# Kernel tuning notes

Measured on AMD Instinct MI355X. Metric: run time of the kernel, lower is better.

The kernel has to match this reference:

```python
import jax, jax.numpy as jnp
import numpy as np

T, IN, OUT = 16384, 4096, 4096


def setup_inputs() -> dict:
    key = jax.random.key(0)
    k1, k2, k3, k4, k5 = jax.random.split(key, 5)
    x = jax.random.randint(k1, (T, IN), -128, 128, dtype=jnp.int32)      # int8-valued activations
    weight = jax.random.randint(k2, (OUT, IN), -128, 128, dtype=jnp.int32)  # int8-valued weights
    bias = jax.random.randint(k3, (OUT,), -128, 128, dtype=jnp.int32)    # int8-valued bias
    # requant scales: alpha = a_scale*w_scale/o_scale, beta = b_scale/o_scale
    alpha = jax.random.uniform(k4, (1,), jnp.float32, 1e-4, 1e-3)
    beta = jax.random.uniform(k5, (1,), jnp.float32, 0.5, 1.5)
    return {"x": x, "weight": weight, "bias": bias, "alpha": alpha, "beta": beta}


def reference(x, weight, bias, alpha, beta):
    # INT8 GEMM with int32 accumulation: acc[t,o] = sum_i x[t,i] * W[o,i]
    acc = jnp.einsum('ti,oi->to', x, weight,
                     preferred_element_type=jnp.int32)  # [T, OUT] int32
    # inline dequant + bias + requant epilogue
    y = acc.astype(jnp.float32) * alpha + bias.astype(jnp.float32) * beta
    # round and saturate to int8 output (W8A8B8O8)
    out = jnp.clip(jnp.round(y), -128.0, 127.0).astype(jnp.int8)
    return out
```

## Files before the change

kernel.cpp:

```cpp
#include <hip/hip_runtime.h>
#include <stdint.h>

constexpr int T_DIM   = 16384;
constexpr int IN_DIM  = 4096;
constexpr int OUT_DIM = 4096;

using int32x4 = __attribute__((ext_vector_type(4))) int;

#define GLOAD_LDS16(g, l)                                                     \
    __builtin_amdgcn_global_load_lds(                                         \
        (const __attribute__((address_space(1))) void*)(uintptr_t)(g),        \
        (__attribute__((address_space(3))) void*)(uintptr_t)(l), 16, 0, 0)

__global__ void pack_swz(const int* __restrict__ src, int8_t* __restrict__ dst,
                         int rows, int cols) {
    int64_t tid = (int64_t)blockIdx.x * blockDim.x + threadIdx.x;
    int64_t nchunks = (int64_t)rows * (cols / 16);
    if (tid >= nchunks) return;
    int row  = (int)(tid / (cols / 16));
    int cidx = (int)(tid % (cols / 16));
    const int32x4* s4 =
        reinterpret_cast<const int32x4*>(src + (int64_t)row * cols + (cidx << 4));
    uint32_t p[4];
#pragma unroll
    for (int v = 0; v < 4; ++v) {
        int32x4 t = s4[v];
        p[v] = (uint32_t)(t[0] & 0xff) | ((uint32_t)(t[1] & 0xff) << 8) |
               ((uint32_t)(t[2] & 0xff) << 16) | ((uint32_t)(t[3] & 0xff) << 24);
    }
    int cs = (cidx & ~7) | ((cidx & 7) ^ (row & 7));
    *reinterpret_cast<int32x4*>(dst + (int64_t)row * cols + (cs << 4)) =
        *reinterpret_cast<int32x4*>(p);
}

constexpr int BM = 256, BN = 256, BK = 128;
constexpr int NT    = IN_DIM / BK;
constexpr int ATILE = BM * BK;
constexpr int BUFSZ = 2 * ATILE;

__global__ __launch_bounds__(512, 2)
void gemm_i8_8p(const int8_t* __restrict__ x8, const int8_t* __restrict__ w8,
                const int* __restrict__ bias, const float* __restrict__ alphap,
                const float* __restrict__ betap, int* __restrict__ out) {
    __shared__ __align__(16) int8_t lds[2 * BUFSZ];

    const int tid  = threadIdx.x;
    const int lane = tid & 63;
    const int wid  = tid >> 6;
    const int wr   = wid >> 2;
    const int wc   = wid & 3;

    const int nwg = gridDim.x;
    const int cpx = nwg >> 3;
    const int bid = blockIdx.x;
    const int swz = (bid & 7) * cpx + (bid >> 3);
    const int bm  = swz >> 4;
    const int bn  = swz & 15;
    const int brow = bm * BM;
    const int bcol = bn * BN;

    const float alpha = *alphap;
    const float beta  = *betap;

    const int g = lane >> 4;
    const int r = lane & 15;

    const int8_t* pA[4];
    const int8_t* pB[4];
    int dA[4], dB[4];
#pragma unroll
    for (int l = 0; l < 4; ++l) {
        const int off = l * 8192 + tid * 16;
        const int row = off >> 7, in = off & 127;
        pA[l] = x8 + (int64_t)(brow + row) * IN_DIM + in;
        pB[l] = w8 + (int64_t)(bcol + row) * IN_DIM + in;
        dA[l] = off;
        dB[l] = ATILE + off;
    }

    int aoff[8], boff[4];
#pragma unroll
    for (int m = 0; m < 8; ++m) {
        const int row = wr * 128 + m * 16 + r;
        aoff[m] = row * BK + ((g ^ (row & 7)) << 4);
    }
#pragma unroll
    for (int n = 0; n < 4; ++n) {
        const int row = wc * 64 + n * 16 + r;
        boff[n] = ATILE + row * BK + ((g ^ (row & 7)) << 4);
    }

    int32x4 acc[8][4] = {};

#define STAGE8(DSTB)                                                          \
    do {                                                                      \
        int8_t* nb = lds + (DSTB) * BUFSZ;                                    \
        _Pragma("unroll") for (int l = 0; l < 4; ++l) {                       \
            GLOAD_LDS16(pA[l], nb + dA[l]);                                   \
            GLOAD_LDS16(pB[l], nb + dB[l]);                                   \
            pA[l] += BK; pB[l] += BK;                                         \
        }                                                                     \
    } while (0)

#define TILE(RB, SB, PF, LAST)                                                \
    do {                                                                      \
        const int8_t* rb = lds + (RB) * BUFSZ;                                \
        if (PF) STAGE8(SB);                                                   \
        int32x4 af[8], bf[4];                                                 \
                                                                  \
        _Pragma("unroll") for (int n = 0; n < 4; ++n)                         \
            bf[n] = *reinterpret_cast<const int32x4*>(rb + boff[n]);          \
        _Pragma("unroll") for (int m = 0; m < 8; ++m)                         \
            af[m] = *reinterpret_cast<const int32x4*>(rb + aoff[m]);          \
        __builtin_amdgcn_s_setprio(1);                                        \
        _Pragma("unroll") for (int m = 0; m < 8; ++m)                         \
            _Pragma("unroll") for (int n = 0; n < 4; ++n)                     \
                acc[m][n] = __builtin_amdgcn_mfma_i32_16x16x64_i8(            \
                    af[m], bf[n], acc[m][n], 0, 0, 0);                        \
        __builtin_amdgcn_s_setprio(0);                                        \
                                                     \
        _Pragma("unroll") for (int n = 0; n < 4; ++n)                         \
            bf[n] = *reinterpret_cast<const int32x4*>(rb + (boff[n] ^ 64));   \
        _Pragma("unroll") for (int m = 0; m < 8; ++m)                         \
            af[m] = *reinterpret_cast<const int32x4*>(rb + (aoff[m] ^ 64));   \
        __builtin_amdgcn_s_setprio(1);                                        \
        _Pragma("unroll") for (int m = 0; m < 8; ++m)                         \
            _Pragma("unroll") for (int n = 0; n < 4; ++n)                     \
                acc[m][n] = __builtin_amdgcn_mfma_i32_16x16x64_i8(            \
                    af[m], bf[n], acc[m][n], 0, 0, 0);                        \
        __builtin_amdgcn_s_setprio(0);                                        \
        if (!(LAST)) {                                                        \
            asm volatile("s_waitcnt vmcnt(0)" ::: "memory");                  \
            __builtin_amdgcn_s_barrier();                                     \
            asm volatile("" ::: "memory");                                    \
        }                                                                     \
    } while (0)

    STAGE8(0);
    asm volatile("s_waitcnt vmcnt(0)" ::: "memory");
    __builtin_amdgcn_s_barrier();
    asm volatile("" ::: "memory");

#pragma unroll 1
    for (int tt = 0; tt < NT - 2; tt += 2) {
        TILE(0, 1, true, false);
        TILE(1, 0, true, false);
    }
    TILE(0, 1, true,  false);
    TILE(1, 0, false, true);
#undef TILE
#undef STAGE8

    const int r4 = (lane >> 4) * 4;
    const int cl = lane & 15;
#pragma unroll
    for (int n = 0; n < 4; ++n) {
        const int col = bcol + wc * 64 + n * 16 + cl;
        const float bterm = (float)bias[col] * beta;
#pragma unroll
        for (int m = 0; m < 8; ++m) {
            const int row0 = brow + wr * 128 + m * 16 + r4;
#pragma unroll
            for (int j = 0; j < 4; ++j) {
                float y = (float)acc[m][n][j] * alpha + bterm;
                y = rintf(y);
                y = fminf(fmaxf(y, -128.0f), 127.0f);
                out[(int64_t)(row0 + j) * OUT_DIM + col] = (int)y;
            }
        }
    }
}

__global__ __launch_bounds__(256)
void gemm_i8_fb(const int* __restrict__ x32, const int* __restrict__ w32,
                const int* __restrict__ bias, const float* __restrict__ alphap,
                const float* __restrict__ betap, int* __restrict__ out) {
    constexpr int FBM = 128, FBK = 128;
    __shared__ int8_t lA[FBM * FBK];
    __shared__ int8_t lB[FBM * FBK];

    const int tid  = threadIdx.x;
    const int wid  = tid >> 6;
    const int lane = tid & 63;
    const int nwg = gridDim.x;
    const int cpx = nwg >> 3;
    const int bid = blockIdx.x;
    const int swz = (bid & 7) * cpx + (bid >> 3);
    const int brow = (swz >> 5) * FBM;
    const int bcol = (swz & 31) * FBM;
    const int wr = wid >> 1, wc = wid & 1;
    const float alpha = *alphap;
    const float beta  = *betap;

    int32x4 acc[4][4] = {};
    for (int kt = 0; kt < IN_DIM / FBK; ++kt) {
        const int64_t kbase = (int64_t)kt * FBK;
#pragma unroll
        for (int q = 0; q < 4; ++q) {
            const int off = wid * 4096 + q * 1024 + lane * 16;
            const int row = off >> 7;
            const int k   = off & 127;
            const int* ga = x32 + (int64_t)(brow + row) * IN_DIM + kbase + k;
            const int* gb = w32 + (int64_t)(bcol + row) * IN_DIM + kbase + k;
            uint32_t pa[4], pb[4];
#pragma unroll
            for (int v = 0; v < 4; ++v) {
                int32x4 ta = reinterpret_cast<const int32x4*>(ga)[v];
                int32x4 tb = reinterpret_cast<const int32x4*>(gb)[v];
                pa[v] = (uint32_t)(ta[0] & 0xff) | ((uint32_t)(ta[1] & 0xff) << 8) |
                        ((uint32_t)(ta[2] & 0xff) << 16) | ((uint32_t)(ta[3] & 0xff) << 24);
                pb[v] = (uint32_t)(tb[0] & 0xff) | ((uint32_t)(tb[1] & 0xff) << 8) |
                        ((uint32_t)(tb[2] & 0xff) << 16) | ((uint32_t)(tb[3] & 0xff) << 24);
            }
            const int sc = ((k >> 4) ^ (row & 7)) << 4;
            *reinterpret_cast<int32x4*>(lA + row * FBK + sc) = *reinterpret_cast<int32x4*>(pa);
            *reinterpret_cast<int32x4*>(lB + row * FBK + sc) = *reinterpret_cast<int32x4*>(pb);
        }
        __syncthreads();
#pragma unroll
        for (int ks = 0; ks < 2; ++ks) {
            const int gg = lane >> 4, rr = lane & 15;
            const int lc = ks * 4 + gg;
            int32x4 af[4], bf[4];
#pragma unroll
            for (int m = 0; m < 4; ++m) {
                const int row = wr * 64 + m * 16 + rr;
                af[m] = *reinterpret_cast<const int32x4*>(lA + row * FBK + ((lc ^ (row & 7)) << 4));
            }
#pragma unroll
            for (int n = 0; n < 4; ++n) {
                const int row = wc * 64 + n * 16 + rr;
                bf[n] = *reinterpret_cast<const int32x4*>(lB + row * FBK + ((lc ^ (row & 7)) << 4));
            }
#pragma unroll
            for (int m = 0; m < 4; ++m)
#pragma unroll
                for (int n = 0; n < 4; ++n)
                    acc[m][n] = __builtin_amdgcn_mfma_i32_16x16x64_i8(af[m], bf[n], acc[m][n], 0, 0, 0);
        }
        __syncthreads();
    }
    const int r4 = (lane >> 4) * 4;
    const int cl = lane & 15;
#pragma unroll
    for (int n = 0; n < 4; ++n) {
        const int col = bcol + wc * 64 + n * 16 + cl;
        const float bterm = (float)bias[col] * beta;
#pragma unroll
        for (int m = 0; m < 4; ++m) {
            const int row0 = brow + wr * 64 + m * 16 + r4;
#pragma unroll
            for (int j = 0; j < 4; ++j) {
                float y = (float)acc[m][n][j] * alpha + bterm;
                y = rintf(y);
                y = fminf(fmaxf(y, -128.0f), 127.0f);
                out[(int64_t)(row0 + j) * OUT_DIM + col] = (int)y;
            }
        }
    }
}

extern "C" void kernel_launch(void* const* d_in, const int* in_sizes, int n_in,
                              void* d_out, int out_size, void* d_ws, size_t ws_size,
                              hipStream_t stream) {
    const int*   x     = (const int*)d_in[0];
    const int*   w     = (const int*)d_in[1];
    const int*   bias  = (const int*)d_in[2];
    const float* alpha = (const float*)d_in[3];
    const float* beta  = (const float*)d_in[4];
    int*         out   = (int*)d_out;

    const size_t need = (size_t)T_DIM * IN_DIM + (size_t)OUT_DIM * IN_DIM;

    if (ws_size >= need) {
        int8_t* x8 = (int8_t*)d_ws;
        int8_t* w8 = x8 + (size_t)T_DIM * IN_DIM;
        {
            int64_t nch = (int64_t)T_DIM * (IN_DIM / 16);
            pack_swz<<<(int)((nch + 255) / 256), 256, 0, stream>>>(x, x8, T_DIM, IN_DIM);
        }
        {
            int64_t nch = (int64_t)OUT_DIM * (IN_DIM / 16);
            pack_swz<<<(int)((nch + 255) / 256), 256, 0, stream>>>(w, w8, OUT_DIM, IN_DIM);
        }
        const int grid = (T_DIM / BM) * (OUT_DIM / BN);
        gemm_i8_8p<<<grid, 512, 0, stream>>>(x8, w8, bias, alpha, beta, out);
    } else {
        const int grid = (T_DIM / 128) * (OUT_DIM / 128);
        gemm_i8_fb<<<grid, 256, 0, stream>>>(x, w, bias, alpha, beta, out);
    }
}
```

Baseline: 383.2 us.

## Shrink GEMM tile to 256x128x64 for higher occupancy with matching swizzle

Changes the main int8 GEMM tile from 256x256 with K-step 128 to 256x128 with K-step 64, so each wave holds a 4x4 accumulator grid instead of 8x4. Launch bounds rise to 4 blocks per CU. The pack kernel's LDS bank swizzle is rewritten for 64-byte rows. The aim is to cut LDS and register use so more waves hide latency, at the cost of more barriers, twice as many K iterations, and less data reuse per tile.

```diff
diff --git a/kernel.cpp b/kernel.cpp
--- a/kernel.cpp
+++ b/kernel.cpp
@@ -28,18 +28,19 @@
         p[v] = (uint32_t)(t[0] & 0xff) | ((uint32_t)(t[1] & 0xff) << 8) |
                ((uint32_t)(t[2] & 0xff) << 16) | ((uint32_t)(t[3] & 0xff) << 24);
     }
-    int cs = (cidx & ~7) | ((cidx & 7) ^ (row & 7));
+    int cs = (cidx & ~3) | ((cidx & 3) ^ ((row >> 1) & 3));
     *reinterpret_cast<int32x4*>(dst + (int64_t)row * cols + (cs << 4)) =
         *reinterpret_cast<int32x4*>(p);
 }
 
-constexpr int BM = 256, BN = 256, BK = 128;
-constexpr int NT    = IN_DIM / BK;
-constexpr int ATILE = BM * BK;
-constexpr int BUFSZ = 2 * ATILE;
-
-__global__ __launch_bounds__(512, 2)
-void gemm_i8_8p(const int8_t* __restrict__ x8, const int8_t* __restrict__ w8,
+constexpr int BM = 256, BN = 128, BK = 64;
+constexpr int NT     = IN_DIM / BK;
+constexpr int ATILE  = BM * BK;
+constexpr int BTILE  = BN * BK;
+constexpr int BUFSZ  = ATILE + BTILE;
+
+__global__ __launch_bounds__(512, 4)
+void gemm_i8_oc(const int8_t* __restrict__ x8, const int8_t* __restrict__ w8,
                 const int* __restrict__ bias, const float* __restrict__ alphap,
                 const float* __restrict__ betap, int* __restrict__ out) {
     __shared__ __align__(16) int8_t lds[2 * BUFSZ];
@@ -47,15 +48,15 @@
     const int tid  = threadIdx.x;
     const int lane = tid & 63;
     const int wid  = tid >> 6;
-    const int wr   = wid >> 2;
-    const int wc   = wid & 3;
+    const int wr   = wid >> 1;
+    const int wc   = wid & 1;
 
     const int nwg = gridDim.x;
     const int cpx = nwg >> 3;
     const int bid = blockIdx.x;
     const int swz = (bid & 7) * cpx + (bid >> 3);
-    const int bm  = swz >> 4;
-    const int bn  = swz & 15;
+    const int bm  = swz >> 5;
+    const int bn  = swz & 31;
     const int brow = bm * BM;
     const int bcol = bn * BN;
 
@@ -65,66 +66,48 @@
     const int g = lane >> 4;
     const int r = lane & 15;
 
-    const int8_t* pA[4];
-    const int8_t* pB[4];
-    int dA[4], dB[4];
-#pragma unroll
-    for (int l = 0; l < 4; ++l) {
-        const int off = l * 8192 + tid * 16;
-        const int row = off >> 7, in = off & 127;
-        pA[l] = x8 + (int64_t)(brow + row) * IN_DIM + in;
-        pB[l] = w8 + (int64_t)(bcol + row) * IN_DIM + in;
-        dA[l] = off;
-        dB[l] = ATILE + off;
-    }
-
-    int aoff[8], boff[4];
-#pragma unroll
-    for (int m = 0; m < 8; ++m) {
-        const int row = wr * 128 + m * 16 + r;
-        aoff[m] = row * BK + ((g ^ (row & 7)) << 4);
+    const int offA0 = tid * 16;
+    const int offA1 = 8192 + tid * 16;
+    const int offB  = tid * 16;
+    const int8_t* pA0 = x8 + (int64_t)(brow + (offA0 >> 6)) * IN_DIM + (offA0 & 63);
+    const int8_t* pA1 = x8 + (int64_t)(brow + (offA1 >> 6)) * IN_DIM + (offA1 & 63);
+    const int8_t* pB0 = w8 + (int64_t)(bcol + (offB  >> 6)) * IN_DIM + (offB  & 63);
+    const int dA0 = offA0, dA1 = offA1, dB0 = ATILE + offB;
+
+    int aoff[4], boff[4];
+#pragma unroll
+    for (int m = 0; m < 4; ++m) {
+        const int row = wr * 64 + m * 16 + r;
+        aoff[m] = row * BK + ((g ^ ((row >> 1) & 3)) << 4);
     }
 #pragma unroll
     for (int n = 0; n < 4; ++n) {
         const int row = wc * 64 + n * 16 + r;
-        boff[n] = ATILE + row * BK + ((g ^ (row & 7)) << 4);
-    }
-
-    int32x4 acc[8][4] = {};
-
-#define STAGE8(DSTB)                                                          \
+        boff[n] = ATILE + row * BK + ((g ^ ((row >> 1) & 3)) << 4);
+    }
+
+    int32x4 acc[4][4] = {};
+
+#define STAGE3(DSTB)                                                          \
     do {                                                                      \
         int8_t* nb = lds + (DSTB) * BUFSZ;                                    \
-        _Pragma("unroll") for (int l = 0; l < 4; ++l) {                       \
-            GLOAD_LDS16(pA[l], nb + dA[l]);                                   \
-            GLOAD_LDS16(pB[l], nb + dB[l]);                                   \
-            pA[l] += BK; pB[l] += BK;                                         \
-        }                                                                     \
+        GLOAD_LDS16(pA0, nb + dA0);                                           \
+        GLOAD_LDS16(pA1, nb + dA1);                                           \
+        GLOAD_LDS16(pB0, nb + dB0);                                           \
+        pA0 += BK; pA1 += BK; pB0 += BK;                                      \
     } while (0)
 
 #define TILE(RB, SB, PF, LAST)                                                \
     do {                                                                      \
+        if (PF) STAGE3(SB);                                                   \
         const int8_t* rb = lds + (RB) * BUFSZ;                                \
-        if (PF) STAGE8(SB);                                                   \
-        int32x4 af[8], bf[4];                                                 \
-                                                                  \
+        int32x4 af[4], bf[4];                                                 \
         _Pragma("unroll") for (int n = 0; n < 4; ++n)                         \
             bf[n] = *reinterpret_cast<const int32x4*>(rb + boff[n]);          \
-        _Pragma("unroll") for (int m = 0; m < 8; ++m)                         \
+        _Pragma("unroll") for (int m = 0; m < 4; ++m)                         \
             af[m] = *reinterpret_cast<const int32x4*>(rb + aoff[m]);          \
         __builtin_amdgcn_s_setprio(1);                                        \
-        _Pragma("unroll") for (int m = 0; m < 8; ++m)                         \
-            _Pragma("unroll") for (int n = 0; n < 4; ++n)                     \
-                acc[m][n] = __builtin_amdgcn_mfma_i32_16x16x64_i8(            \
-                    af[m], bf[n], acc[m][n], 0, 0, 0);                        \
-        __builtin_amdgcn_s_setprio(0);                                        \
-                                                     \
-        _Pragma("unroll") for (int n = 0; n < 4; ++n)                         \
-            bf[n] = *reinterpret_cast<const int32x4*>(rb + (boff[n] ^ 64));   \
-        _Pragma("unroll") for (int m = 0; m < 8; ++m)                         \
-            af[m] = *reinterpret_cast<const int32x4*>(rb + (aoff[m] ^ 64));   \
-        __builtin_amdgcn_s_setprio(1);                                        \
-        _Pragma("unroll") for (int m = 0; m < 8; ++m)                         \
+        _Pragma("unroll") for (int m = 0; m < 4; ++m)                         \
             _Pragma("unroll") for (int n = 0; n < 4; ++n)                     \
                 acc[m][n] = __builtin_amdgcn_mfma_i32_16x16x64_i8(            \
                     af[m], bf[n], acc[m][n], 0, 0, 0);                        \
@@ -136,7 +119,7 @@
         }                                                                     \
     } while (0)
 
-    STAGE8(0);
+    STAGE3(0);
     asm volatile("s_waitcnt vmcnt(0)" ::: "memory");
     __builtin_amdgcn_s_barrier();
     asm volatile("" ::: "memory");
@@ -149,7 +132,7 @@
     TILE(0, 1, true,  false);
     TILE(1, 0, false, true);
 #undef TILE
-#undef STAGE8
+#undef STAGE3
 
     const int r4 = (lane >> 4) * 4;
     const int cl = lane & 15;
@@ -158,8 +141,8 @@
         const int col = bcol + wc * 64 + n * 16 + cl;
         const float bterm = (float)bias[col] * beta;
 #pragma unroll
-        for (int m = 0; m < 8; ++m) {
-            const int row0 = brow + wr * 128 + m * 16 + r4;
+        for (int m = 0; m < 4; ++m) {
+            const int row0 = brow + wr * 64 + m * 16 + r4;
 #pragma unroll
             for (int j = 0; j < 4; ++j) {
                 float y = (float)acc[m][n][j] * alpha + bterm;
@@ -284,7 +267,7 @@
             pack_swz<<<(int)((nch + 255) / 256), 256, 0, stream>>>(w, w8, OUT_DIM, IN_DIM);
         }
         const int grid = (T_DIM / BM) * (OUT_DIM / BN);
-        gemm_i8_8p<<<grid, 512, 0, stream>>>(x8, w8, bias, alpha, beta, out);
+        gemm_i8_oc<<<grid, 512, 0, stream>>>(x8, w8, bias, alpha, beta, out);
     } else {
         const int grid = (T_DIM / 128) * (OUT_DIM / 128);
         gemm_i8_fb<<<grid, 256, 0, stream>>>(x, w, bias, alpha, beta, out);
```

After: 418.7 us, median of 4. +9.3%, slower.

## Load pre-packed MFMA-fragment weights directly to registers, halve K tile

Applied to the files above, without the earlier changes.

The weight matrix is now pre-packed into MFMA-fragment order, so each lane loads its B operand straight from global memory into registers with double-buffered prefetch, bypassing LDS. Only the activation tile goes through LDS, and BK is halved to 64 with a matching swizzle, so LDS use per block drops. The aim is to cut LDS traffic and shared-memory bank pressure for B. In exchange there are twice as many barrier-synchronised iterations with less MFMA work per barrier, and each B fragment is reloaded from global/L2 by every block that uses it.

```diff
diff --git a/kernel.cpp b/kernel.cpp
--- a/kernel.cpp
+++ b/kernel.cpp
@@ -12,8 +12,8 @@
         (const __attribute__((address_space(1))) void*)(uintptr_t)(g),        \
         (__attribute__((address_space(3))) void*)(uintptr_t)(l), 16, 0, 0)
 
-__global__ void pack_swz(const int* __restrict__ src, int8_t* __restrict__ dst,
-                         int rows, int cols) {
+__global__ void pack_a(const int* __restrict__ src, int8_t* __restrict__ dst,
+                       int rows, int cols) {
     int64_t tid = (int64_t)blockIdx.x * blockDim.x + threadIdx.x;
     int64_t nchunks = (int64_t)rows * (cols / 16);
     if (tid >= nchunks) return;
@@ -28,21 +28,46 @@
         p[v] = (uint32_t)(t[0] & 0xff) | ((uint32_t)(t[1] & 0xff) << 8) |
                ((uint32_t)(t[2] & 0xff) << 16) | ((uint32_t)(t[3] & 0xff) << 24);
     }
-    int cs = (cidx & ~7) | ((cidx & 7) ^ (row & 7));
+    int cs = (cidx & ~3) | ((cidx & 3) ^ ((row >> 1) & 3));
     *reinterpret_cast<int32x4*>(dst + (int64_t)row * cols + (cs << 4)) =
         *reinterpret_cast<int32x4*>(p);
 }
 
-constexpr int BM = 256, BN = 256, BK = 128;
+__global__ void pack_b(const int* __restrict__ src, int8_t* __restrict__ dst,
+                       int rows, int cols) {
+    int64_t tid = (int64_t)blockIdx.x * blockDim.x + threadIdx.x;
+    int64_t nchunks = (int64_t)rows * (cols / 16);
+    if (tid >= nchunks) return;
+    int o  = (int)(tid / (cols / 16));
+    int kc = (int)(tid % (cols / 16));
+    const int32x4* s4 =
+        reinterpret_cast<const int32x4*>(src + (int64_t)o * cols + (kc << 4));
+    uint32_t p[4];
+#pragma unroll
+    for (int v = 0; v < 4; ++v) {
+        int32x4 t = s4[v];
+        p[v] = (uint32_t)(t[0] & 0xff) | ((uint32_t)(t[1] & 0xff) << 8) |
+               ((uint32_t)(t[2] & 0xff) << 16) | ((uint32_t)(t[3] & 0xff) << 24);
+    }
+    const int o_tile = o >> 4;
+    const int k_tile = kc >> 2;
+    const int g      = kc & 3;
+    const int r      = o & 15;
+    const int64_t off =
+        ((int64_t)o_tile * (cols >> 6) + k_tile) * 1024 + g * 256 + r * 16;
+    *reinterpret_cast<int32x4*>(dst + off) = *reinterpret_cast<int32x4*>(p);
+}
+
+constexpr int BM = 256, BN = 256, BK = 64;
 constexpr int NT    = IN_DIM / BK;
 constexpr int ATILE = BM * BK;
-constexpr int BUFSZ = 2 * ATILE;
+constexpr int NKT   = IN_DIM / 64;
 
 __global__ __launch_bounds__(512, 2)
-void gemm_i8_8p(const int8_t* __restrict__ x8, const int8_t* __restrict__ w8,
+void gemm_i8_bb(const int8_t* __restrict__ x8, const int8_t* __restrict__ w8p,
                 const int* __restrict__ bias, const float* __restrict__ alphap,
                 const float* __restrict__ betap, int* __restrict__ out) {
-    __shared__ __align__(16) int8_t lds[2 * BUFSZ];
+    __shared__ __align__(16) int8_t lds[2 * ATILE];
 
     const int tid  = threadIdx.x;
     const int lane = tid & 63;
@@ -65,69 +90,57 @@
     const int g = lane >> 4;
     const int r = lane & 15;
 
-    const int8_t* pA[4];
+    const int offA0 = tid * 16;
+    const int offA1 = 8192 + tid * 16;
+    const int8_t* pA0 = x8 + (int64_t)(brow + (offA0 >> 6)) * IN_DIM + (offA0 & 63);
+    const int8_t* pA1 = x8 + (int64_t)(brow + (offA1 >> 6)) * IN_DIM + (offA1 & 63);
+    const int dA0 = offA0, dA1 = offA1;
+
     const int8_t* pB[4];
-    int dA[4], dB[4];
-#pragma unroll
-    for (int l = 0; l < 4; ++l) {
-        const int off = l * 8192 + tid * 16;
-        const int row = off >> 7, in = off & 127;
-        pA[l] = x8 + (int64_t)(brow + row) * IN_DIM + in;
-        pB[l] = w8 + (int64_t)(bcol + row) * IN_DIM + in;
-        dA[l] = off;
-        dB[l] = ATILE + off;
-    }
-
-    int aoff[8], boff[4];
+#pragma unroll
+    for (int n = 0; n < 4; ++n) {
+        const int o_tile = (bcol >> 4) + wc * 4 + n;
+        pB[n] = w8p + (int64_t)o_tile * NKT * 1024 + lane * 16;
+    }
+
+    int aoff[8];
 #pragma unroll
     for (int m = 0; m < 8; ++m) {
         const int row = wr * 128 + m * 16 + r;
-        aoff[m] = row * BK + ((g ^ (row & 7)) << 4);
-    }
-#pragma unroll
-    for (int n = 0; n < 4; ++n) {
-        const int row = wc * 64 + n * 16 + r;
-        boff[n] = ATILE + row * BK + ((g ^ (row & 7)) << 4);
+        aoff[m] = row * BK + ((g ^ ((row >> 1) & 3)) << 4);
     }
 
     int32x4 acc[8][4] = {};
-
-#define STAGE8(DSTB)                                                          \
+    int32x4 b0[4], b1[4];
+
+#define STAGE_A(DSTB)                                                         \
     do {                                                                      \
-        int8_t* nb = lds + (DSTB) * BUFSZ;                                    \
-        _Pragma("unroll") for (int l = 0; l < 4; ++l) {                       \
-            GLOAD_LDS16(pA[l], nb + dA[l]);                                   \
-            GLOAD_LDS16(pB[l], nb + dB[l]);                                   \
-            pA[l] += BK; pB[l] += BK;                                         \
+        int8_t* nb = lds + (DSTB) * ATILE;                                    \
+        GLOAD_LDS16(pA0, nb + dA0);                                           \
+        GLOAD_LDS16(pA1, nb + dA1);                                           \
+        pA0 += BK; pA1 += BK;                                                 \
+    } while (0)
+
+#define LOAD_B(DST)                                                           \
+    do {                                                                      \
+        _Pragma("unroll") for (int n = 0; n < 4; ++n) {                       \
+            DST[n] = *reinterpret_cast<const int32x4*>(pB[n]);                \
+            pB[n] += 1024;                                                    \
         }                                                                     \
     } while (0)
 
-#define TILE(RB, SB, PF, LAST)                                                \
+#define TILE(RB, SB, PF, BC, BNX, LAST)                                       \
     do {                                                                      \
-        const int8_t* rb = lds + (RB) * BUFSZ;                                \
-        if (PF) STAGE8(SB);                                                   \
-        int32x4 af[8], bf[4];                                                 \
-                                                                  \
-        _Pragma("unroll") for (int n = 0; n < 4; ++n)                         \
-            bf[n] = *reinterpret_cast<const int32x4*>(rb + boff[n]);          \
+        if (PF) { STAGE_A(SB); LOAD_B(BNX); }                                 \
+        const int8_t* rb = lds + (RB) * ATILE;                                \
+        int32x4 af[8];                                                        \
         _Pragma("unroll") for (int m = 0; m < 8; ++m)                         \
             af[m] = *reinterpret_cast<const int32x4*>(rb + aoff[m]);          \
         __builtin_amdgcn_s_setprio(1);                                        \
         _Pragma("unroll") for (int m = 0; m < 8; ++m)                         \
             _Pragma("unroll") for (int n = 0; n < 4; ++n)                     \
                 acc[m][n] = __builtin_amdgcn_mfma_i32_16x16x64_i8(            \
-                    af[m], bf[n], acc[m][n], 0, 0, 0);                        \
-        __builtin_amdgcn_s_setprio(0);                                        \
-                                                     \
-        _Pragma("unroll") for (int n = 0; n < 4; ++n)                         \
-            bf[n] = *reinterpret_cast<const int32x4*>(rb + (boff[n] ^ 64));   \
-        _Pragma("unroll") for (int m = 0; m < 8; ++m)                         \
-            af[m] = *reinterpret_cast<const int32x4*>(rb + (aoff[m] ^ 64));   \
-        __builtin_amdgcn_s_setprio(1);                                        \
-        _Pragma("unroll") for (int m = 0; m < 8; ++m)                         \
-            _Pragma("unroll") for (int n = 0; n < 4; ++n)                     \
-                acc[m][n] = __builtin_amdgcn_mfma_i32_16x16x64_i8(            \
-                    af[m], bf[n], acc[m][n], 0, 0, 0);                        \
+                    af[m], BC[n], acc[m][n], 0, 0, 0);                        \
         __builtin_amdgcn_s_setprio(0);                                        \
         if (!(LAST)) {                                                        \
             asm volatile("s_waitcnt vmcnt(0)" ::: "memory");                  \
@@ -136,20 +149,22 @@
         }                                                                     \
     } while (0)
 
-    STAGE8(0);
+    STAGE_A(0);
+    LOAD_B(b0);
     asm volatile("s_waitcnt vmcnt(0)" ::: "memory");
     __builtin_amdgcn_s_barrier();
     asm volatile("" ::: "memory");
 
 #pragma unroll 1
     for (int tt = 0; tt < NT - 2; tt += 2) {
-        TILE(0, 1, true, false);
-        TILE(1, 0, true, false);
-    }
-    TILE(0, 1, true,  false);
-    TILE(1, 0, false, true);
+        TILE(0, 1, true, b0, b1, false);
+        TILE(1, 0, true, b1, b0, false);
+    }
+    TILE(0, 1, true,  b0, b1, false);
+    TILE(1, 0, false, b1, b0, true);
 #undef TILE
-#undef STAGE8
+#undef LOAD_B
+#undef STAGE_A
 
     const int r4 = (lane >> 4) * 4;
     const int cl = lane & 15;
@@ -273,18 +288,18 @@
     const size_t need = (size_t)T_DIM * IN_DIM + (size_t)OUT_DIM * IN_DIM;
 
     if (ws_size >= need) {
-        int8_t* x8 = (int8_t*)d_ws;
-        int8_t* w8 = x8 + (size_t)T_DIM * IN_DIM;
+        int8_t* x8  = (int8_t*)d_ws;
+        int8_t* w8p = x8 + (size_t)T_DIM * IN_DIM;
         {
             int64_t nch = (int64_t)T_DIM * (IN_DIM / 16);
-            pack_swz<<<(int)((nch + 255) / 256), 256, 0, stream>>>(x, x8, T_DIM, IN_DIM);
+            pack_a<<<(int)((nch + 255) / 256), 256, 0, stream>>>(x, x8, T_DIM, IN_DIM);
         }
         {
             int64_t nch = (int64_t)OUT_DIM * (IN_DIM / 16);
-            pack_swz<<<(int)((nch + 255) / 256), 256, 0, stream>>>(w, w8, OUT_DIM, IN_DIM);
+            pack_b<<<(int)((nch + 255) / 256), 256, 0, stream>>>(w, w8p, OUT_DIM, IN_DIM);
         }
         const int grid = (T_DIM / BM) * (OUT_DIM / BN);
-        gemm_i8_8p<<<grid, 512, 0, stream>>>(x8, w8, bias, alpha, beta, out);
+        gemm_i8_bb<<<grid, 512, 0, stream>>>(x8, w8p, bias, alpha, beta, out);
     } else {
         const int grid = (T_DIM / 128) * (OUT_DIM / 128);
         gemm_i8_fb<<<grid, 256, 0, stream>>>(x, w, bias, alpha, beta, out);
```

Result: slower. 468.0 us (+22.1%).
